# Optimization experiments

Measured on AMD Instinct MI355X. Metric: run time of the kernel, lower is better.

Reference implementation:

```python
import jax, jax.numpy as jnp
import numpy as np

N_NODES = 50000
N_EDGES = 1600000
N_GRAPHS = 512
L = 3
D = 128
E_FEAT = 16
BN_EPS = 1e-5


def setup_inputs() -> dict:
    key = jax.random.key(0)
    ks = jax.random.split(key, 16)
    s = 0.05
    inp = {
        "x": jax.random.normal(ks[0], (N_NODES, D), jnp.float32),
        "edge_attr": jax.random.normal(ks[1], (N_EDGES, E_FEAT), jnp.float32),
        "el_W": jax.random.normal(ks[2], (L, E_FEAT, D), jnp.float32) * s,
        "el_b": jax.random.normal(ks[3], (L, D), jnp.float32) * s,
        "W1": jax.random.normal(ks[4], (L, D, D), jnp.float32) * s,
        "b1": jax.random.normal(ks[5], (L, D), jnp.float32) * s,
        "bn_g": jnp.ones((L, D), jnp.float32),
        "bn_b": jnp.zeros((L, D), jnp.float32),
        "bn_mean": jnp.zeros((L, D), jnp.float32),
        "bn_var": jnp.ones((L, D), jnp.float32),
        "W2": jax.random.normal(ks[6], (L, D, D), jnp.float32) * s,
        "b2": jax.random.normal(ks[7], (L, D), jnp.float32) * s,
        "lin1_W": jax.random.normal(ks[8], (L * D, L * D), jnp.float32) * s,
        "lin1_b": jax.random.normal(ks[9], (L * D,), jnp.float32) * s,
        "lin2_W": jax.random.normal(ks[10], (L * D, 1), jnp.float32) * s,
        "lin2_b": jax.random.normal(ks[11], (1,), jnp.float32) * s,
        "edge_index": jax.random.randint(ks[12], (2, N_EDGES), 0, N_NODES, jnp.int64),
        "batch": jnp.sort(jax.random.randint(ks[13], (N_NODES,), 0, N_GRAPHS, jnp.int64)),
    }
    return inp


def reference(x, edge_attr, el_W, el_b, W1, b1, bn_g, bn_b, bn_mean, bn_var,
              W2, b2, lin1_W, lin1_b, lin2_W, lin2_b, edge_index, batch):
    src, dst = edge_index[0], edge_index[1]  # x_j = x[src], aggregated into dst
    h = x
    pools = []
    for l in range(L):
        # GINEConv message: relu(x_j + Linear(edge_attr))
        e = edge_attr @ el_W[l] + el_b[l]            # [E, D]
        m = jax.nn.relu(h[src] + e)                  # [E, D]  (dominant traffic)
        aggr = jax.ops.segment_sum(m, dst, num_segments=N_NODES)  # scatter-add
        z = h + aggr                                 # (1+eps)*x_i + aggr, eps=0
        # MLP: Linear -> BatchNorm (eval) -> ReLU -> Linear
        z = z @ W1[l] + b1[l]
        z = (z - bn_mean[l]) * (bn_g[l] / jnp.sqrt(bn_var[l] + BN_EPS)) + bn_b[l]
        z = jax.nn.relu(z)
        z = z @ W2[l] + b2[l]
        h = jax.nn.relu(z)                           # outer F.relu in GINENet
        pools.append(jax.ops.segment_sum(h, batch, num_segments=N_GRAPHS))
    g = jnp.concatenate(pools, axis=1)               # [G, L*D]
    g = jax.nn.relu(g @ lin1_W + lin1_b)             # dropout inactive (eval)
    return g @ lin2_W + lin2_b                       # [G, 1]
```

## Files before the change

### kernel.cpp

```cpp
#include <hip/hip_runtime.h>

#define N_NODES   50000
#define N_EDGES   1600000
#define N_GRAPHS  512
#define LAYERS    3
#define D         128
#define EF        16
#define BN_EPS    1e-5f

#define SCAN_CH   256
#define SCAN_NB   ((N_NODES + SCAN_CH - 1) / SCAN_CH)

typedef unsigned int u32;
typedef short bf16x8 __attribute__((ext_vector_type(8)));
typedef float f32x4 __attribute__((ext_vector_type(4)));

__device__ __forceinline__ unsigned short f2bf(float f) {
    unsigned u = __builtin_bit_cast(unsigned, f);
    u += 0x7FFF + ((u >> 16) & 1);
    return (unsigned short)(u >> 16);
}

__device__ __forceinline__ float bf2f(unsigned short u) {
    return __builtin_bit_cast(float, (unsigned)u << 16);
}

__device__ __forceinline__ u32 pack_bf2(float x, float y) {
    return ((u32)f2bf(x)) | ((u32)f2bf(y) << 16);
}

__global__ __launch_bounds__(256) void hist_kernel(
    const int* __restrict__ dst, int* __restrict__ counts)
{
    int e = blockIdx.x * 256 + threadIdx.x;
    atomicAdd(&counts[dst[e]], 1);
}

__global__ __launch_bounds__(256) void scan1_kernel(
    const int* __restrict__ counts, int* __restrict__ blocksum)
{
    const int t = threadIdx.x;
    const int i = blockIdx.x * SCAN_CH + t;
    int v = (i < N_NODES) ? counts[i] : 0;
    #pragma unroll
    for (int off = 32; off > 0; off >>= 1)
        v += __shfl_down(v, off);
    __shared__ int ws[4];
    if ((t & 63) == 0) ws[t >> 6] = v;
    __syncthreads();
    if (t == 0) blocksum[blockIdx.x] = ws[0] + ws[1] + ws[2] + ws[3];
}

__global__ __launch_bounds__(256) void scan2_kernel(
    const int* __restrict__ blocksum, int* __restrict__ blockbase)
{
    __shared__ int s[256];
    const int t = threadIdx.x;
    int v = (t < SCAN_NB) ? blocksum[t] : 0;
    s[t] = v;
    __syncthreads();
    for (int off = 1; off < 256; off <<= 1) {
        int u = (t >= off) ? s[t - off] : 0;
        __syncthreads();
        s[t] += u;
        __syncthreads();
    }
    if (t < SCAN_NB) blockbase[t] = s[t] - v;
}

__global__ __launch_bounds__(256) void scan3_kernel(
    const int* __restrict__ counts, const int* __restrict__ blockbase,
    int* __restrict__ offsets, int* __restrict__ cursor)
{
    __shared__ int s[256];
    const int t = threadIdx.x;
    const int i = blockIdx.x * SCAN_CH + t;
    int v = (i < N_NODES) ? counts[i] : 0;
    s[t] = v;
    __syncthreads();
    for (int off = 1; off < 256; off <<= 1) {
        int u = (t >= off) ? s[t - off] : 0;
        __syncthreads();
        s[t] += u;
        __syncthreads();
    }
    if (i < N_NODES) {
        const int base = blockbase[blockIdx.x];
        const int excl = base + s[t] - v;
        offsets[i] = excl;
        cursor[i]  = excl;
        if (i == N_NODES - 1) offsets[N_NODES] = base + s[t];
    }
}

__global__ __launch_bounds__(256) void scatter_kernel(
    const int* __restrict__ src, const int* __restrict__ dst,
    const float* __restrict__ edge_attr,
    int* __restrict__ cursor, int* __restrict__ sorted_src,
    uint4* __restrict__ sorted_eah)
{
    int e = blockIdx.x * 256 + threadIdx.x;
    int d = dst[e];
    int pos = atomicAdd(&cursor[d], 1);
    sorted_src[pos] = src[e];
    const float4* ea = (const float4*)(edge_attr + (size_t)e * EF);
    float4 a0 = ea[0], a1 = ea[1], a2 = ea[2], a3 = ea[3];
    uint4 o0, o1;
    o0.x = pack_bf2(a0.x, a0.y); o0.y = pack_bf2(a0.z, a0.w);
    o0.z = pack_bf2(a1.x, a1.y); o0.w = pack_bf2(a1.z, a1.w);
    o1.x = pack_bf2(a2.x, a2.y); o1.y = pack_bf2(a2.z, a2.w);
    o1.z = pack_bf2(a3.x, a3.y); o1.w = pack_bf2(a3.z, a3.w);
    sorted_eah[(size_t)pos * 2]     = o0;
    sorted_eah[(size_t)pos * 2 + 1] = o1;
}

__global__ __launch_bounds__(512) void goff_kernel(
    const int* __restrict__ batch, int* __restrict__ goff,
    u32* __restrict__ xb_dummy, u32* __restrict__ hA_dummy)
{
    const int g = threadIdx.x;
    if (g < 64) {
        xb_dummy[g] = 0xFF7FFF7Fu;
        hA_dummy[g] = 0xFF7FFF7Fu;
    }
    int lo = 0, hi = N_NODES;
    while (lo < hi) {
        int mid = (lo + hi) >> 1;
        if (batch[mid] < g) lo = mid + 1; else hi = mid;
    }
    goff[g] = lo;
    if (g == 0) goff[N_GRAPHS] = N_NODES;
}

__global__ __launch_bounds__(256) void wprep_kernel(
    const float* __restrict__ W1, const float* __restrict__ W2,
    unsigned short* __restrict__ Wt)
{
    const int matid = blockIdx.x;
    const int l = matid >> 1;
    const float* srcm = (matid & 1) ? (W2 + (size_t)l * D * D)
                                    : (W1 + (size_t)l * D * D);
    unsigned short* out = Wt + (size_t)matid * D * D;
    for (int i = 0; i < 64; ++i) {
        int idx = threadIdx.x + i * 256;
        int k = idx >> 7, n = idx & 127;
        out[n * D + k] = f2bf(srcm[idx]);
    }
}

__global__ __launch_bounds__(512) void elprep_kernel(
    const float* __restrict__ elW, const float* __restrict__ elb,
    uint4* __restrict__ elWf)
{
    const int l    = blockIdx.x;
    const int t    = threadIdx.x >> 6;
    const int lane = threadIdx.x & 63;
    const int q = lane >> 4, c = lane & 15;
    const float* W = elW + (size_t)l * EF * D;
    unsigned short h[8];
    #pragma unroll
    for (int i = 0; i < 8; ++i) {
        int k = q * 8 + i;
        float v = 0.f;
        if (q < 2)                 v = W[k * D + t * 16 + c];
        else if (q == 2 && i == 0) v = elb[l * D + t * 16 + c];
        h[i] = f2bf(v);
    }
    uint4 o;
    o.x = (u32)h[0] | ((u32)h[1] << 16);
    o.y = (u32)h[2] | ((u32)h[3] << 16);
    o.z = (u32)h[4] | ((u32)h[5] << 16);
    o.w = (u32)h[6] | ((u32)h[7] << 16);
    elWf[((size_t)l * 8 + t) * 64 + lane] = o;
}

__global__ __launch_bounds__(256) void xprep_kernel(
    const float* __restrict__ x, unsigned short* __restrict__ xb)
{
    int i = blockIdx.x * 256 + threadIdx.x;
    xb[i] = f2bf(x[i]);
}

__global__ __launch_bounds__(128) void aggr_kernel(
    const unsigned short* __restrict__ h_b,
    const uint4* __restrict__ sorted_ea,
    const int*   __restrict__ sorted_src,
    const int*   __restrict__ offsets,
    const uint4* __restrict__ elWf,
    u32* __restrict__ zin_b)
{
    const int tid  = threadIdx.x;
    const int wv   = tid >> 6;
    const int lane = tid & 63;
    const int q    = lane >> 4;
    const int c    = lane & 15;
    const int n    = blockIdx.x;

    bf16x8 bfr[8];
    #pragma unroll
    for (int t = 0; t < 8; ++t)
        bfr[t] = __builtin_bit_cast(bf16x8, elWf[t * 64 + lane]);

    const u32 mand = (q < 2) ? 0xFFFFFFFFu : 0u;
    const u32 mor0 = (q == 2) ? 0x3F80u : 0u;

    const int beg = offsets[n];
    const int end = offsets[n + 1];
    const int nch = (end - beg + 15) >> 4;

    float acc[8];
    #pragma unroll
    for (int t = 0; t < 8; ++t) acc[t] = 0.f;

    const f32x4 zero4 = (f32x4){0.f, 0.f, 0.f, 0.f};

    for (int ch = wv; ch < nch; ch += 2) {
        const int e0 = beg + ch * 16;

        uint4 araw = sorted_ea[(size_t)(e0 + c) * 2 + (q & 1)];
        uint4 aw;
        aw.x = (araw.x & mand) | mor0;
        aw.y =  araw.y & mand;
        aw.z =  araw.z & mand;
        aw.w =  araw.w & mand;
        const bf16x8 afr = __builtin_bit_cast(bf16x8, aw);

        const int er0 = e0 + q * 4;
        int s0 = (er0 + 0 < end) ? sorted_src[er0 + 0] : N_NODES;
        int s1 = (er0 + 1 < end) ? sorted_src[er0 + 1] : N_NODES;
        int s2 = (er0 + 2 < end) ? sorted_src[er0 + 2] : N_NODES;
        int s3 = (er0 + 3 < end) ? sorted_src[er0 + 3] : N_NODES;
        const unsigned short* hr0 = h_b + (size_t)s0 * D + c;
        const unsigned short* hr1 = h_b + (size_t)s1 * D + c;
        const unsigned short* hr2 = h_b + (size_t)s2 * D + c;
        const unsigned short* hr3 = h_b + (size_t)s3 * D + c;

        unsigned short hv0[8], hv1[8], hv2[8], hv3[8];
        #pragma unroll
        for (int t = 0; t < 8; ++t) {
            hv0[t] = hr0[t * 16];
            hv1[t] = hr1[t * 16];
            hv2[t] = hr2[t * 16];
            hv3[t] = hr3[t * 16];
        }

        #pragma unroll
        for (int t = 0; t < 8; ++t) {
            f32x4 C = __builtin_amdgcn_mfma_f32_16x16x32_bf16(
                afr, bfr[t], zero4, 0, 0, 0);
            float v0 = fmaxf(C[0] + bf2f(hv0[t]), 0.f);
            float v1 = fmaxf(C[1] + bf2f(hv1[t]), 0.f);
            float v2 = fmaxf(C[2] + bf2f(hv2[t]), 0.f);
            float v3 = fmaxf(C[3] + bf2f(hv3[t]), 0.f);
            acc[t] += (v0 + v1) + (v2 + v3);
        }
    }

    #pragma unroll
    for (int t = 0; t < 8; ++t) {
        float v = acc[t];
        v += __shfl_xor(v, 16);
        v += __shfl_xor(v, 32);
        acc[t] = v;
    }

    __shared__ float sums[2][128];
    if (lane < 32) {
        const int tb = (lane >> 4) * 4;
        #pragma unroll
        for (int j = 0; j < 4; ++j)
            sums[wv][(tb + j) * 16 + c] = acc[tb + j];
    }
    __syncthreads();

    if (wv == 0) {
        float2 r0 = ((const float2*)sums[0])[lane];
        float2 r1 = ((const float2*)sums[1])[lane];
        const u32 hs2 = *(const u32*)(h_b + (size_t)n * D + 2 * lane);
        const float hA = __builtin_bit_cast(float, hs2 << 16);
        const float hB = __builtin_bit_cast(float, hs2 & 0xFFFF0000u);
        zin_b[(size_t)n * 64 + lane] =
            pack_bf2(hA + r0.x + r1.x, hB + r0.y + r1.y);
    }
}

__global__ __launch_bounds__(128) void node_mlp(
    const unsigned short* __restrict__ zin_b,
    const unsigned short* __restrict__ W1t,
    const float* __restrict__ b1,
    const float* __restrict__ bng, const float* __restrict__ bnb,
    const float* __restrict__ bnm, const float* __restrict__ bnv,
    const unsigned short* __restrict__ W2t,
    const float* __restrict__ b2,
    unsigned short* __restrict__ hout_b)
{
    __shared__ unsigned short zmid[64 * 136];
    __shared__ float scale_s[128], shift_s[128], b2_s[128];

    const int tid  = threadIdx.x;
    const int wv   = tid >> 6;
    const int lane = tid & 63;
    const int q    = lane >> 4;
    const int m    = lane & 15;
    const int node0 = blockIdx.x * 64;

    {
        float sc = bng[tid] * rsqrtf(bnv[tid] + BN_EPS);
        scale_s[tid] = sc;
        shift_s[tid] = b1[tid] * sc + bnb[tid] - bnm[tid] * sc;
        b2_s[tid]    = b2[tid];
    }

    bf16x8 a[2][4];
    #pragma unroll
    for (int sub = 0; sub < 2; ++sub) {
        int node = node0 + wv * 32 + sub * 16 + m;
        if (node >= N_NODES) node = N_NODES - 1;
        const uint4* zrow = (const uint4*)(zin_b + (size_t)node * D);
        #pragma unroll
        for (int k = 0; k < 4; ++k)
            a[sub][k] = __builtin_bit_cast(bf16x8, zrow[k * 4 + q]);
    }

    f32x4 acc[2][8];
    #pragma unroll
    for (int s2 = 0; s2 < 2; ++s2)
        #pragma unroll
        for (int t = 0; t < 8; ++t)
            acc[s2][t] = (f32x4){0.f, 0.f, 0.f, 0.f};

    __syncthreads();

    #pragma unroll
    for (int t = 0; t < 8; ++t) {
        const unsigned short* wrow = W1t + (size_t)(t * 16 + m) * D;
        bf16x8 bfr[4];
        #pragma unroll
        for (int k = 0; k < 4; ++k)
            bfr[k] = __builtin_bit_cast(bf16x8, *(const uint4*)&wrow[k * 32 + q * 8]);
        #pragma unroll
        for (int sub = 0; sub < 2; ++sub) {
            acc[sub][t] = __builtin_amdgcn_mfma_f32_16x16x32_bf16(a[sub][0], bfr[0], acc[sub][t], 0, 0, 0);
            acc[sub][t] = __builtin_amdgcn_mfma_f32_16x16x32_bf16(a[sub][1], bfr[1], acc[sub][t], 0, 0, 0);
            acc[sub][t] = __builtin_amdgcn_mfma_f32_16x16x32_bf16(a[sub][2], bfr[2], acc[sub][t], 0, 0, 0);
            acc[sub][t] = __builtin_amdgcn_mfma_f32_16x16x32_bf16(a[sub][3], bfr[3], acc[sub][t], 0, 0, 0);
        }
    }

    #pragma unroll
    for (int sub = 0; sub < 2; ++sub)
        #pragma unroll
        for (int t = 0; t < 8; ++t) {
            int col = t * 16 + m;
            float sc = scale_s[col], sh = shift_s[col];
            #pragma unroll
            for (int rr = 0; rr < 4; ++rr) {
                float v = fmaxf(acc[sub][t][rr] * sc + sh, 0.f);
                int row = wv * 32 + sub * 16 + q * 4 + rr;
                zmid[row * 136 + col] = f2bf(v);
            }
        }

    __syncthreads();

    bf16x8 a2[2][4];
    #pragma unroll
    for (int sub = 0; sub < 2; ++sub) {
        const unsigned short* zr = &zmid[(wv * 32 + sub * 16 + m) * 136];
        #pragma unroll
        for (int k = 0; k < 4; ++k)
            a2[sub][k] = __builtin_bit_cast(bf16x8, *(const uint4*)&zr[k * 32 + q * 8]);
    }

    #pragma unroll
    for (int s2 = 0; s2 < 2; ++s2)
        #pragma unroll
        for (int t = 0; t < 8; ++t)
            acc[s2][t] = (f32x4){0.f, 0.f, 0.f, 0.f};

    #pragma unroll
    for (int t = 0; t < 8; ++t) {
        const unsigned short* wrow = W2t + (size_t)(t * 16 + m) * D;
        bf16x8 bfr[4];
        #pragma unroll
        for (int k = 0; k < 4; ++k)
            bfr[k] = __builtin_bit_cast(bf16x8, *(const uint4*)&wrow[k * 32 + q * 8]);
        #pragma unroll
        for (int sub = 0; sub < 2; ++sub) {
            acc[sub][t] = __builtin_amdgcn_mfma_f32_16x16x32_bf16(a2[sub][0], bfr[0], acc[sub][t], 0, 0, 0);
            acc[sub][t] = __builtin_amdgcn_mfma_f32_16x16x32_bf16(a2[sub][1], bfr[1], acc[sub][t], 0, 0, 0);
            acc[sub][t] = __builtin_amdgcn_mfma_f32_16x16x32_bf16(a2[sub][2], bfr[2], acc[sub][t], 0, 0, 0);
            acc[sub][t] = __builtin_amdgcn_mfma_f32_16x16x32_bf16(a2[sub][3], bfr[3], acc[sub][t], 0, 0, 0);
        }
    }

    #pragma unroll
    for (int sub = 0; sub < 2; ++sub)
        #pragma unroll
        for (int rr = 0; rr < 4; ++rr) {
            int node = node0 + wv * 32 + sub * 16 + q * 4 + rr;
            if (node < N_NODES) {
                unsigned short* hrow = hout_b + (size_t)node * D;
                #pragma unroll
                for (int t = 0; t < 8; ++t) {
                    int col = t * 16 + m;
                    hrow[col] = f2bf(fmaxf(acc[sub][t][rr] + b2_s[col], 0.f));
                }
            }
        }
}

__global__ __launch_bounds__(512) void pool_kernel(
    const unsigned short* __restrict__ hout_b, const int* __restrict__ goff,
    float* __restrict__ pool, int layer_off)
{
    __shared__ float part[3][128];
    const int g = blockIdx.x;
    const int j = threadIdx.x & 127;
    const int grp = threadIdx.x >> 7;
    const int beg = goff[g], end = goff[g + 1];
    const int len = end - beg;
    const int ch  = (len + 3) >> 2;
    int lo = beg + grp * ch;
    int hi = lo + ch;
    if (hi > end) hi = end;
    float acc = 0.0f;
    for (int r = lo; r < hi; ++r)
        acc += bf2f(hout_b[(size_t)r * D + j]);
    if (grp) part[grp - 1][j] = acc;
    __syncthreads();
    if (grp == 0)
        pool[g * (LAYERS * D) + layer_off + j] =
            acc + part[0][j] + part[1][j] + part[2][j];
}

__global__ __launch_bounds__(384) void head_kernel(
    const float* __restrict__ pool,
    const float* __restrict__ lin1W,
    const float* __restrict__ lin1b,
    const float* __restrict__ lin2W,
    const float* __restrict__ lin2b,
    float*       __restrict__ out)
{
    __shared__ float gs[LAYERS * D];
    __shared__ float red[LAYERS * D];
    const int g   = blockIdx.x;
    const int tid = threadIdx.x;
    gs[tid] = pool[g * (LAYERS * D) + tid];
    __syncthreads();

    float acc = lin1b[tid];
    #pragma unroll 4
    for (int k = 0; k < LAYERS * D; ++k)
        acc = fmaf(gs[k], lin1W[k * (LAYERS * D) + tid], acc);
    acc = fmaxf(acc, 0.0f);
    float p = acc * lin2W[tid];

    red[tid] = p;
    __syncthreads();
    if (tid < 128) red[tid] = red[tid] + red[tid + 128] + red[tid + 256];
    __syncthreads();
    if (tid < 64) {
        float v = red[tid] + red[tid + 64];
        v += __shfl_down(v, 32);
        v += __shfl_down(v, 16);
        v += __shfl_down(v, 8);
        v += __shfl_down(v, 4);
        v += __shfl_down(v, 2);
        v += __shfl_down(v, 1);
        if (tid == 0) out[g] = v + lin2b[0];
    }
}

extern "C" void kernel_launch(void* const* d_in, const int* in_sizes, int n_in,
                              void* d_out, int out_size, void* d_ws, size_t ws_size,
                              hipStream_t stream)
{
    const float* x         = (const float*)d_in[0];
    const float* edge_attr = (const float*)d_in[1];
    const float* elW       = (const float*)d_in[2];
    const float* elb       = (const float*)d_in[3];
    const float* W1        = (const float*)d_in[4];
    const float* b1        = (const float*)d_in[5];
    const float* bn_g      = (const float*)d_in[6];
    const float* bn_b      = (const float*)d_in[7];
    const float* bn_mean   = (const float*)d_in[8];
    const float* bn_var    = (const float*)d_in[9];
    const float* W2        = (const float*)d_in[10];
    const float* b2        = (const float*)d_in[11];
    const float* lin1W     = (const float*)d_in[12];
    const float* lin1b     = (const float*)d_in[13];
    const float* lin2W     = (const float*)d_in[14];
    const float* lin2b     = (const float*)d_in[15];
    const int*   ei        = (const int*)d_in[16];
    const int*   batch     = (const int*)d_in[17];
    const int*   src = ei;
    const int*   dst = ei + N_EDGES;

    float*          pool       = (float*)d_ws;
    unsigned short* xb         = (unsigned short*)(pool + (size_t)N_GRAPHS * LAYERS * D);
    unsigned short* hA_b       = xb   + (size_t)(N_NODES + 1) * D;
    unsigned short* zin_b      = hA_b + (size_t)(N_NODES + 1) * D;
    unsigned short* Wt         = zin_b + (size_t)N_NODES * D;
    uint4*          elWf       = (uint4*)(Wt + 6 * D * D);
    u32*            sorted_eah = (u32*)(elWf + LAYERS * 8 * 64);
    int*            sorted_src = (int*)(sorted_eah + (size_t)(N_EDGES + 16) * 8);
    int*            counts     = sorted_src + N_EDGES + 16;
    int*            offsets    = counts + N_NODES;
    int*            cursor     = offsets + N_NODES + 4;
    int*            goff       = cursor + N_NODES + 4;
    int*            blocksum   = goff + N_GRAPHS + 4;
    int*            blockbase  = blocksum + SCAN_NB + 4;

    hipMemsetAsync(counts, 0, (size_t)N_NODES * sizeof(int), stream);
    hipMemsetAsync(sorted_eah + (size_t)N_EDGES * 8, 0, 16 * 32, stream);
    hipMemsetAsync(sorted_src + N_EDGES, 0, 16 * sizeof(int), stream);

    wprep_kernel<<<6, 256, 0, stream>>>(W1, W2, Wt);
    elprep_kernel<<<LAYERS, 512, 0, stream>>>(elW, elb, elWf);
    xprep_kernel<<<(N_NODES * D) / 256, 256, 0, stream>>>(x, xb);
    goff_kernel<<<1, 512, 0, stream>>>(batch, goff,
        (u32*)(xb + (size_t)N_NODES * D), (u32*)(hA_b + (size_t)N_NODES * D));
    hist_kernel<<<N_EDGES / 256, 256, 0, stream>>>(dst, counts);
    scan1_kernel<<<SCAN_NB, 256, 0, stream>>>(counts, blocksum);
    scan2_kernel<<<1, 256, 0, stream>>>(blocksum, blockbase);
    scan3_kernel<<<SCAN_NB, 256, 0, stream>>>(counts, blockbase, offsets, cursor);
    scatter_kernel<<<N_EDGES / 256, 256, 0, stream>>>(
        src, dst, edge_attr, cursor, sorted_src, (uint4*)sorted_eah);

    const unsigned short* hin_b = xb;
    for (int l = 0; l < LAYERS; ++l) {
        aggr_kernel<<<N_NODES, 128, 0, stream>>>(
            hin_b, (const uint4*)sorted_eah, sorted_src, offsets,
            elWf + (size_t)l * 8 * 64, (u32*)zin_b);
        node_mlp<<<(N_NODES + 63) / 64, 128, 0, stream>>>(
            zin_b,
            Wt + (size_t)(l * 2)     * D * D, b1 + l * D,
            bn_g + l * D, bn_b + l * D, bn_mean + l * D, bn_var + l * D,
            Wt + (size_t)(l * 2 + 1) * D * D, b2 + l * D,
            hA_b);
        pool_kernel<<<N_GRAPHS, 512, 0, stream>>>(hA_b, goff, pool, l * D);
        hin_b = hA_b;
    }

    head_kernel<<<N_GRAPHS, LAYERS * D, 0, stream>>>(
        pool, lin1W, lin1b, lin2W, lin2b, (float*)d_out);
}
```

Before: 869.1 us.

## Balance edge aggregation across waves with segmented reduction and atomic flushes

Replaces the one-block-per-node aggregation with a fixed grid of waves, each owning an equal contiguous range of dst-sorted edge chunks. Each wave runs a segmented reduction and flushes partial sums to an fp32 buffer with atomics at node boundaries, using a precomputed start node per wave. The MFMA edge-feature result is staged in LDS so each lane can gather a contiguous bf16 pair per edge, and the residual add of h moves into node_mlp. The aim is to remove load imbalance from skewed node degrees and per-node launch overhead, at the cost of a per-layer memset, fp32 atomics and twice the bytes for the intermediate buffer.

```diff
diff --git a/kernel.cpp b/kernel.cpp
--- a/kernel.cpp
+++ b/kernel.cpp
@@ -11,6 +11,12 @@
 #define SCAN_CH   256
 #define SCAN_NB   ((N_NODES + SCAN_CH - 1) / SCAN_CH)
 
+#define NCHUNK    (N_EDGES / 16)
+#define AGGR_BLK  1024
+#define AGGR_WPB  4
+#define NWAVES    (AGGR_BLK * AGGR_WPB)
+#define ELDS_STR  130
+
 typedef unsigned int u32;
 typedef short bf16x8 __attribute__((ext_vector_type(8)));
 typedef float f32x4 __attribute__((ext_vector_type(4)));
@@ -23,6 +29,13 @@
 
 __device__ __forceinline__ float bf2f(unsigned short u) {
     return __builtin_bit_cast(float, (unsigned)u << 16);
+}
+
+__device__ __forceinline__ float lo16f(u32 u) {
+    return __builtin_bit_cast(float, u << 16);
+}
+__device__ __forceinline__ float hi16f(u32 u) {
+    return __builtin_bit_cast(float, u & 0xFFFF0000u);
 }
 
 __device__ __forceinline__ u32 pack_bf2(float x, float y) {
@@ -91,6 +104,21 @@
         cursor[i]  = excl;
         if (i == N_NODES - 1) offsets[N_NODES] = base + s[t];
     }
+}
+
+__global__ __launch_bounds__(256) void wstart_kernel(
+    const int* __restrict__ offsets, int* __restrict__ wstart)
+{
+    const int w = blockIdx.x * 256 + threadIdx.x;
+    const int qc = NCHUNK / NWAVES, rc = NCHUNK % NWAVES;
+    const int c0 = w * qc + (w < rc ? w : rc);
+    const int elo = c0 * 16;
+    int lo = 0, hi = N_NODES - 1;
+    while (lo < hi) {
+        int mid = (lo + hi + 1) >> 1;
+        if (offsets[mid] <= elo) lo = mid; else hi = mid - 1;
+    }
+    wstart[w] = lo;
 }
 
 __global__ __launch_bounds__(256) void scatter_kernel(
@@ -115,14 +143,9 @@
 }
 
 __global__ __launch_bounds__(512) void goff_kernel(
-    const int* __restrict__ batch, int* __restrict__ goff,
-    u32* __restrict__ xb_dummy, u32* __restrict__ hA_dummy)
+    const int* __restrict__ batch, int* __restrict__ goff)
 {
     const int g = threadIdx.x;
-    if (g < 64) {
-        xb_dummy[g] = 0xFF7FFF7Fu;
-        hA_dummy[g] = 0xFF7FFF7Fu;
-    }
     int lo = 0, hi = N_NODES;
     while (lo < hi) {
         int mid = (lo + hi) >> 1;
@@ -181,20 +204,25 @@
     xb[i] = f2bf(x[i]);
 }
 
-__global__ __launch_bounds__(128) void aggr_kernel(
+__global__ __launch_bounds__(256) void aggr_kernel(
     const unsigned short* __restrict__ h_b,
     const uint4* __restrict__ sorted_ea,
     const int*   __restrict__ sorted_src,
     const int*   __restrict__ offsets,
+    const int*   __restrict__ wstart,
     const uint4* __restrict__ elWf,
-    u32* __restrict__ zin_b)
-{
+    float* __restrict__ zin_f)
+{
+    __shared__ float e_lds_all[AGGR_WPB][16 * ELDS_STR];
     const int tid  = threadIdx.x;
-    const int wv   = tid >> 6;
+    const int wv   = __builtin_amdgcn_readfirstlane(tid >> 6);
     const int lane = tid & 63;
     const int q    = lane >> 4;
     const int c    = lane & 15;
-    const int n    = blockIdx.x;
+    const int j0   = lane * 2;
+    const int w    = blockIdx.x * AGGR_WPB + wv;
+
+    float* e_lds = e_lds_all[wv];
 
     bf16x8 bfr[8];
     #pragma unroll
@@ -204,19 +232,33 @@
     const u32 mand = (q < 2) ? 0xFFFFFFFFu : 0u;
     const u32 mor0 = (q == 2) ? 0x3F80u : 0u;
 
-    const int beg = offsets[n];
-    const int end = offsets[n + 1];
-    const int nch = (end - beg + 15) >> 4;
-
-    float acc[8];
-    #pragma unroll
-    for (int t = 0; t < 8; ++t) acc[t] = 0.f;
-
+    const int qc = NCHUNK / NWAVES, rc = NCHUNK % NWAVES;
+    const int c0 = w * qc + (w < rc ? w : rc);
+    const int cn = qc + (w < rc ? 1 : 0);
+    const int e_lo = c0 * 16;
+    const int e_hi = (c0 + cn) * 16;
+
+    int cur = wstart[w];
+    int nxt = offsets[cur + 1];
+    float accA = 0.f, accB = 0.f;
     const f32x4 zero4 = (f32x4){0.f, 0.f, 0.f, 0.f};
 
-    for (int ch = wv; ch < nch; ch += 2) {
-        const int e0 = beg + ch * 16;
-
+#define PROC(EIDX, SVAL)                                                     \
+    {                                                                        \
+        const int e_ = e0 + (EIDX);                                          \
+        if (e_ >= nxt) {                                                     \
+            atomicAdd(&zin_f[(size_t)cur * D + j0],     accA);               \
+            atomicAdd(&zin_f[(size_t)cur * D + j0 + 1], accB);               \
+            accA = 0.f; accB = 0.f;                                          \
+            do { ++cur; nxt = offsets[cur + 1]; } while (e_ >= nxt);         \
+        }                                                                    \
+        const u32 hv_ = *(const u32*)(h_b + (size_t)(SVAL) * D + j0);        \
+        const float2 ev_ = *(const float2*)&e_lds[(EIDX) * ELDS_STR + j0];   \
+        accA += fmaxf(ev_.x + lo16f(hv_), 0.f);                              \
+        accB += fmaxf(ev_.y + hi16f(hv_), 0.f);                              \
+    }
+
+    for (int e0 = e_lo; e0 < e_hi; e0 += 16) {
         uint4 araw = sorted_ea[(size_t)(e0 + c) * 2 + (q & 1)];
         uint4 aw;
         aw.x = (araw.x & mand) | mor0;
@@ -225,67 +267,32 @@
         aw.w =  araw.w & mand;
         const bf16x8 afr = __builtin_bit_cast(bf16x8, aw);
 
-        const int er0 = e0 + q * 4;
-        int s0 = (er0 + 0 < end) ? sorted_src[er0 + 0] : N_NODES;
-        int s1 = (er0 + 1 < end) ? sorted_src[er0 + 1] : N_NODES;
-        int s2 = (er0 + 2 < end) ? sorted_src[er0 + 2] : N_NODES;
-        int s3 = (er0 + 3 < end) ? sorted_src[er0 + 3] : N_NODES;
-        const unsigned short* hr0 = h_b + (size_t)s0 * D + c;
-        const unsigned short* hr1 = h_b + (size_t)s1 * D + c;
-        const unsigned short* hr2 = h_b + (size_t)s2 * D + c;
-        const unsigned short* hr3 = h_b + (size_t)s3 * D + c;
-
-        unsigned short hv0[8], hv1[8], hv2[8], hv3[8];
-        #pragma unroll
-        for (int t = 0; t < 8; ++t) {
-            hv0[t] = hr0[t * 16];
-            hv1[t] = hr1[t * 16];
-            hv2[t] = hr2[t * 16];
-            hv3[t] = hr3[t * 16];
-        }
+        const int4* sp = (const int4*)(sorted_src + e0);
+        const int4 s0 = sp[0], s1 = sp[1], s2 = sp[2], s3 = sp[3];
 
         #pragma unroll
         for (int t = 0; t < 8; ++t) {
             f32x4 C = __builtin_amdgcn_mfma_f32_16x16x32_bf16(
                 afr, bfr[t], zero4, 0, 0, 0);
-            float v0 = fmaxf(C[0] + bf2f(hv0[t]), 0.f);
-            float v1 = fmaxf(C[1] + bf2f(hv1[t]), 0.f);
-            float v2 = fmaxf(C[2] + bf2f(hv2[t]), 0.f);
-            float v3 = fmaxf(C[3] + bf2f(hv3[t]), 0.f);
-            acc[t] += (v0 + v1) + (v2 + v3);
+            #pragma unroll
+            for (int rr = 0; rr < 4; ++rr)
+                e_lds[(q * 4 + rr) * ELDS_STR + t * 16 + c] = C[rr];
         }
-    }
-
-    #pragma unroll
-    for (int t = 0; t < 8; ++t) {
-        float v = acc[t];
-        v += __shfl_xor(v, 16);
-        v += __shfl_xor(v, 32);
-        acc[t] = v;
-    }
-
-    __shared__ float sums[2][128];
-    if (lane < 32) {
-        const int tb = (lane >> 4) * 4;
-        #pragma unroll
-        for (int j = 0; j < 4; ++j)
-            sums[wv][(tb + j) * 16 + c] = acc[tb + j];
-    }
-    __syncthreads();
-
-    if (wv == 0) {
-        float2 r0 = ((const float2*)sums[0])[lane];
-        float2 r1 = ((const float2*)sums[1])[lane];
-        const u32 hs2 = *(const u32*)(h_b + (size_t)n * D + 2 * lane);
-        const float hA = __builtin_bit_cast(float, hs2 << 16);
-        const float hB = __builtin_bit_cast(float, hs2 & 0xFFFF0000u);
-        zin_b[(size_t)n * 64 + lane] =
-            pack_bf2(hA + r0.x + r1.x, hB + r0.y + r1.y);
-    }
+
+        PROC(0,  s0.x) PROC(1,  s0.y) PROC(2,  s0.z) PROC(3,  s0.w)
+        PROC(4,  s1.x) PROC(5,  s1.y) PROC(6,  s1.z) PROC(7,  s1.w)
+        PROC(8,  s2.x) PROC(9,  s2.y) PROC(10, s2.z) PROC(11, s2.w)
+        PROC(12, s3.x) PROC(13, s3.y) PROC(14, s3.z) PROC(15, s3.w)
+    }
+#undef PROC
+
+    atomicAdd(&zin_f[(size_t)cur * D + j0],     accA);
+    atomicAdd(&zin_f[(size_t)cur * D + j0 + 1], accB);
 }
 
 __global__ __launch_bounds__(128) void node_mlp(
-    const unsigned short* __restrict__ zin_b,
+    const float* __restrict__ zin_f,
+    const unsigned short* __restrict__ h_in,
     const unsigned short* __restrict__ W1t,
     const float* __restrict__ b1,
     const float* __restrict__ bng, const float* __restrict__ bnb,
@@ -316,10 +323,25 @@
     for (int sub = 0; sub < 2; ++sub) {
         int node = node0 + wv * 32 + sub * 16 + m;
         if (node >= N_NODES) node = N_NODES - 1;
-        const uint4* zrow = (const uint4*)(zin_b + (size_t)node * D);
-        #pragma unroll
-        for (int k = 0; k < 4; ++k)
-            a[sub][k] = __builtin_bit_cast(bf16x8, zrow[k * 4 + q]);
+        const float* zr = zin_f + (size_t)node * D;
+        const unsigned short* hr = h_in + (size_t)node * D;
+        #pragma unroll
+        for (int kk = 0; kk < 4; ++kk) {
+            const int base = kk * 32 + q * 8;
+            float4 z0 = *(const float4*)(zr + base);
+            float4 z1 = *(const float4*)(zr + base + 4);
+            uint4  hv = *(const uint4*)(hr + base);
+            bf16x8 t;
+            t[0] = (short)f2bf(z0.x + lo16f(hv.x));
+            t[1] = (short)f2bf(z0.y + hi16f(hv.x));
+            t[2] = (short)f2bf(z0.z + lo16f(hv.y));
+            t[3] = (short)f2bf(z0.w + hi16f(hv.y));
+            t[4] = (short)f2bf(z1.x + lo16f(hv.z));
+            t[5] = (short)f2bf(z1.y + hi16f(hv.z));
+            t[6] = (short)f2bf(z1.z + lo16f(hv.w));
+            t[7] = (short)f2bf(z1.w + hi16f(hv.w));
+            a[sub][kk] = t;
+        }
     }
 
     f32x4 acc[2][8];
@@ -499,42 +521,42 @@
 
     float*          pool       = (float*)d_ws;
     unsigned short* xb         = (unsigned short*)(pool + (size_t)N_GRAPHS * LAYERS * D);
-    unsigned short* hA_b       = xb   + (size_t)(N_NODES + 1) * D;
-    unsigned short* zin_b      = hA_b + (size_t)(N_NODES + 1) * D;
-    unsigned short* Wt         = zin_b + (size_t)N_NODES * D;
+    unsigned short* hA_b       = xb   + (size_t)N_NODES * D;
+    float*          zin_f      = (float*)(hA_b + (size_t)N_NODES * D);
+    unsigned short* Wt         = (unsigned short*)(zin_f + (size_t)N_NODES * D);
     uint4*          elWf       = (uint4*)(Wt + 6 * D * D);
     u32*            sorted_eah = (u32*)(elWf + LAYERS * 8 * 64);
-    int*            sorted_src = (int*)(sorted_eah + (size_t)(N_EDGES + 16) * 8);
-    int*            counts     = sorted_src + N_EDGES + 16;
+    int*            sorted_src = (int*)(sorted_eah + (size_t)N_EDGES * 8);
+    int*            counts     = sorted_src + N_EDGES;
     int*            offsets    = counts + N_NODES;
     int*            cursor     = offsets + N_NODES + 4;
     int*            goff       = cursor + N_NODES + 4;
     int*            blocksum   = goff + N_GRAPHS + 4;
     int*            blockbase  = blocksum + SCAN_NB + 4;
+    int*            wstart     = blockbase + SCAN_NB + 4;
 
     hipMemsetAsync(counts, 0, (size_t)N_NODES * sizeof(int), stream);
-    hipMemsetAsync(sorted_eah + (size_t)N_EDGES * 8, 0, 16 * 32, stream);
-    hipMemsetAsync(sorted_src + N_EDGES, 0, 16 * sizeof(int), stream);
 
     wprep_kernel<<<6, 256, 0, stream>>>(W1, W2, Wt);
     elprep_kernel<<<LAYERS, 512, 0, stream>>>(elW, elb, elWf);
     xprep_kernel<<<(N_NODES * D) / 256, 256, 0, stream>>>(x, xb);
-    goff_kernel<<<1, 512, 0, stream>>>(batch, goff,
-        (u32*)(xb + (size_t)N_NODES * D), (u32*)(hA_b + (size_t)N_NODES * D));
+    goff_kernel<<<1, 512, 0, stream>>>(batch, goff);
     hist_kernel<<<N_EDGES / 256, 256, 0, stream>>>(dst, counts);
     scan1_kernel<<<SCAN_NB, 256, 0, stream>>>(counts, blocksum);
     scan2_kernel<<<1, 256, 0, stream>>>(blocksum, blockbase);
     scan3_kernel<<<SCAN_NB, 256, 0, stream>>>(counts, blockbase, offsets, cursor);
+    wstart_kernel<<<NWAVES / 256, 256, 0, stream>>>(offsets, wstart);
     scatter_kernel<<<N_EDGES / 256, 256, 0, stream>>>(
         src, dst, edge_attr, cursor, sorted_src, (uint4*)sorted_eah);
 
     const unsigned short* hin_b = xb;
     for (int l = 0; l < LAYERS; ++l) {
-        aggr_kernel<<<N_NODES, 128, 0, stream>>>(
-            hin_b, (const uint4*)sorted_eah, sorted_src, offsets,
-            elWf + (size_t)l * 8 * 64, (u32*)zin_b);
+        hipMemsetAsync(zin_f, 0, (size_t)N_NODES * D * sizeof(float), stream);
+        aggr_kernel<<<AGGR_BLK, 256, 0, stream>>>(
+            hin_b, (const uint4*)sorted_eah, sorted_src, offsets, wstart,
+            elWf + (size_t)l * 8 * 64, zin_f);
         node_mlp<<<(N_NODES + 63) / 64, 128, 0, stream>>>(
-            zin_b,
+            zin_f, hin_b,
             Wt + (size_t)(l * 2)     * D * D, b1 + l * D,
             bn_g + l * D, bn_b + l * D, bn_mean + l * D, bn_var + l * D,
             Wt + (size_t)(l * 2 + 1) * D * D, b2 + l * D,
```

Result: slower. 1.027 ms (+18.2%).
